# Performance work log

Hardware: AMD Instinct MI355X
Metric: run time of the kernel (lower is better)

The kernel has to match this reference:

```python
import jax, jax.numpy as jnp
import numpy as np

B, S, E, H = 2, 2048, 1024, 16
DH = E // H


def setup_inputs() -> dict:
    key = jax.random.key(0)
    ks = jax.random.split(key, 7)
    sc = 1.0 / np.sqrt(E)
    return {
        "x": jax.random.normal(ks[0], (B, S, E), dtype=jnp.float32),
        "Wq": jax.random.uniform(ks[1], (E, E), jnp.float32, -sc, sc),
        "bq": jax.random.uniform(ks[2], (E,), jnp.float32, -sc, sc),
        "Wk": jax.random.uniform(ks[3], (E, E), jnp.float32, -sc, sc),
        "bk": jax.random.uniform(ks[4], (E,), jnp.float32, -sc, sc),
        "Wv": jax.random.uniform(ks[5], (E, E), jnp.float32, -sc, sc),
        "bv": jax.random.uniform(ks[6], (E,), jnp.float32, -sc, sc),
    }


def reference(x, Wq, bq, Wk, bk, Wv, bv):
    b, s, _ = x.shape
    # torch Linear: y = x @ W.T + b
    q = (x @ Wq.T + bq).reshape(b, s, H, DH).transpose(0, 2, 1, 3)  # [B,H,S,Dh]
    k = (x @ Wk.T + bk).reshape(b, s, H, DH).transpose(0, 2, 1, 3)
    v = (x @ Wv.T + bv).reshape(b, s, H, DH).transpose(0, 2, 1, 3)
    # original einsum labels treat axis1 as 's' and axis2 as 'h'/'v':
    # scores: [B, S_q, H, S_k]  (softmax over keys, last axis)
    scores = jnp.einsum('bshd,bsvd->bhsv', q, k) / np.sqrt(DH)
    probs = jax.nn.softmax(scores, axis=-1)
    # out: [B, H, S, Dh] per original label permutation
    out = jnp.einsum('bhsv,bsvd->bshd', probs, v)
    # original reshapes WITHOUT transposing heads back (faithful quirk)
    return out.reshape(b, s, E)
```

## Files before the change

### kernel.cpp

```cpp
#include <hip/hip_runtime.h>
#include <hip/hip_bf16.h>

#define Bb 2
#define Ss 2048
#define Ee 1024
#define Hh 16
#define Dh 64
#define QSCALE 0.18033688011112042f

using u16 = unsigned short;
using u32 = unsigned int;
typedef __attribute__((ext_vector_type(8))) short short8;
typedef __attribute__((ext_vector_type(8))) u16 ushort8;
typedef __attribute__((ext_vector_type(4))) float f32x4;
typedef __attribute__((ext_vector_type(16))) float f32x16;
typedef __attribute__((ext_vector_type(4))) u32 uint4v;

#define GAS __attribute__((address_space(1)))
#define LAS __attribute__((address_space(3)))

__device__ __forceinline__ void gload16(const u16* g, u16* l) {
  __builtin_amdgcn_global_load_lds((const GAS unsigned int*)g,
                                   (LAS unsigned int*)l, 16, 0, 0);
}

__device__ __forceinline__ u16 f2bf(float f) {
  union { float f; unsigned u; } v;
  v.f = f;
  unsigned u = v.u;
  unsigned r = (u + 0x7FFFu + ((u >> 16) & 1u)) >> 16;
  return (u16)r;
}

__global__ __launch_bounds__(256) void cvt_all(
    const float* __restrict__ x, const float* __restrict__ wq,
    const float* __restrict__ wk, const float* __restrict__ wv,
    u16* __restrict__ xo, u16* __restrict__ wqo, u16* __restrict__ wko,
    u16* __restrict__ wvo) {
  const int b = blockIdx.x;
  const float* s;
  u16* d;
  int i;
  if (b < 2048) {
    s = x; d = xo; i = b * 256 + threadIdx.x;
  } else {
    const int wb = b - 2048;
    const int which = wb >> 9;
    s = which == 0 ? wq : (which == 1 ? wk : wv);
    d = which == 0 ? wqo : (which == 1 ? wko : wvo);
    i = (wb & 511) * 256 + threadIdx.x;
  }
  const float* p = s + (size_t)i * 8;
  ushort8 o;
#pragma unroll
  for (int j = 0; j < 8; ++j) o[j] = f2bf(p[j]);
  *(ushort8*)(d + (size_t)i * 8) = o;
}

__global__ __launch_bounds__(256) void qkv_gemm(
    const u16* __restrict__ Xb, const u16* __restrict__ Wcat,
    const float* __restrict__ bq, const float* __restrict__ bk,
    const float* __restrict__ bv,
    u16* __restrict__ Qo, u16* __restrict__ Ko, u16* __restrict__ Vo) {
  __shared__ u16 Ast[128][64];
  __shared__ u16 Bst[128][64];
  const int tid = threadIdx.x;
  const int lane = tid & 63;
  const int w = tid >> 6;
  const int wm = w >> 1, wn = w & 1;
  const int c = lane & 15, g = lane >> 4;
  const int m0 = blockIdx.y * 128;
  const int n0 = blockIdx.x * 128;
  const bool swapv = n0 >= 2048;

  f32x4 acc[4][4] = {};

  for (int kt = 0; kt < 16; ++kt) {
    const int k0 = kt * 64;
    __syncthreads();
#pragma unroll
    for (int i = 0; i < 4; ++i) {
      const int elem = i * 2048 + tid * 8;
      const int row = elem >> 6, col = elem & 63;
      const int lbase = i * 2048 + w * 512;
      gload16(Xb + (size_t)(m0 + row) * 1024 + k0 + col, &Ast[0][0] + lbase);
      gload16(Wcat + (size_t)(n0 + row) * 1024 + k0 + col, &Bst[0][0] + lbase);
    }
    __syncthreads();

#pragma unroll
    for (int ks = 0; ks < 2; ++ks) {
      short8 af[4], bf[4];
#pragma unroll
      for (int mf = 0; mf < 4; ++mf)
        af[mf] = *(const short8*)&Ast[wm * 64 + mf * 16 + c][ks * 32 + g * 8];
#pragma unroll
      for (int nf = 0; nf < 4; ++nf)
        bf[nf] = *(const short8*)&Bst[wn * 64 + nf * 16 + c][ks * 32 + g * 8];
      if (!swapv) {
#pragma unroll
        for (int mf = 0; mf < 4; ++mf)
#pragma unroll
          for (int nf = 0; nf < 4; ++nf)
            acc[mf][nf] = __builtin_amdgcn_mfma_f32_16x16x32_bf16(
                af[mf], bf[nf], acc[mf][nf], 0, 0, 0);
      } else {
#pragma unroll
        for (int mf = 0; mf < 4; ++mf)
#pragma unroll
          for (int nf = 0; nf < 4; ++nf)
            acc[mf][nf] = __builtin_amdgcn_mfma_f32_16x16x32_bf16(
                bf[nf], af[mf], acc[mf][nf], 0, 0, 0);
      }
    }
  }

  if (!swapv) {
    const int which = n0 >> 10;
    u16* Oo = which == 0 ? Qo : Ko;
    const float* bias = which == 0 ? bq : bk;
    const float scl = which == 0 ? QSCALE : 1.0f;
#pragma unroll
    for (int nf = 0; nf < 4; ++nf) {
      const int n = (n0 & 1023) + wn * 64 + nf * 16 + c;
      const float bval = bias[n];
      const int hh = n >> 6, dd = n & 63;
#pragma unroll
      for (int mf = 0; mf < 4; ++mf) {
#pragma unroll
        for (int r = 0; r < 4; ++r) {
          const int m = m0 + wm * 64 + mf * 16 + g * 4 + r;
          const int bb = m >> 11, ss = m & 2047;
          Oo[(((size_t)bb * Hh + hh) * Ss + ss) * Dh + dd] =
              f2bf((acc[mf][nf][r] + bval) * scl);
        }
      }
    }
  } else {
#pragma unroll
    for (int nf = 0; nf < 4; ++nf) {
#pragma unroll
      for (int r = 0; r < 4; ++r) {
        const int n = (n0 - 2048) + wn * 64 + nf * 16 + g * 4 + r;
        const float bval = bv[n];
        const int hh = n >> 6, dd = n & 63;
#pragma unroll
        for (int mf = 0; mf < 4; ++mf) {
          const int m = m0 + wm * 64 + mf * 16 + c;
          const int bb = m >> 11, ss = m & 2047;
          Vo[(((size_t)bb * Hh + hh) * Dh + dd) * Ss + ss] =
              f2bf(acc[mf][nf][r] + bval);
        }
      }
    }
  }
}

__global__ __launch_bounds__(256) void attn(
    const u16* __restrict__ Q, const u16* __restrict__ K,
    const u16* __restrict__ VT, float* __restrict__ out) {
  __shared__ u16 Kst[2][64][64];
  __shared__ u16 Vst[2][64][64];
  __shared__ float l_lds[4][32];
  const int tid = threadIdx.x;
  const int lane = tid & 63;
  const int w = tid >> 6;
  const int c5 = lane & 31, g2 = lane >> 5;
  const int bh = blockIdx.y;
  const int q0 = blockIdx.x * 128;
  const u16* Qb = Q + (size_t)bh * Ss * Dh;
  const u16* Kb = K + (size_t)bh * Ss * Dh;
  const u16* VTb = VT + (size_t)bh * Ss * Dh;

  const int srow = lane >> 3;
  const int scolx = ((lane & 7) * 8) ^ (srow * 8);

  const u16* Qrow = Qb + (size_t)(q0 + w * 32 + c5) * Dh + 8 * g2;
  short8 qf[4];
#pragma unroll
  for (int s = 0; s < 4; ++s) qf[s] = *(const short8*)(Qrow + 16 * s);

#pragma unroll
  for (int p = 0; p < 2; ++p) {
    const int row = w * 8 + srow + p * 32;
    gload16(Kb + (size_t)row * Dh + scolx, &Kst[0][0][0] + w * 512 + p * 2048);
    gload16(VTb + (size_t)row * Ss + scolx, &Vst[0][0][0] + w * 512 + p * 2048);
  }

  f32x16 oacc0 = {}, oacc1 = {};
  float lsum = 0.f;

  for (int kt = 0; kt < 32; ++kt) {
    __syncthreads();
    if (kt < 31) {
      const int k0n = (kt + 1) * 64;
      const int nb = (kt + 1) & 1;
#pragma unroll
      for (int p = 0; p < 2; ++p) {
        const int row = w * 8 + srow + p * 32;
        gload16(Kb + (size_t)(k0n + row) * Dh + scolx,
                &Kst[nb][0][0] + w * 512 + p * 2048);
        gload16(VTb + (size_t)row * Ss + k0n + scolx,
                &Vst[nb][0][0] + w * 512 + p * 2048);
      }
    }
    const char* kbuf = (const char*)&Kst[kt & 1][0][0];
    const char* vbuf = (const char*)&Vst[kt & 1][0][0];
    const int cxor = (c5 & 7) << 4;

    f32x16 sc0 = {}, sc1 = {};
    __builtin_amdgcn_s_setprio(1);
#pragma unroll
    for (int s = 0; s < 4; ++s) {
      const int cb = (32 * s + 16 * g2) ^ cxor;
      short8 kf0 = *(const short8*)(kbuf + c5 * 128 + cb);
      short8 kf1 = *(const short8*)(kbuf + (32 + c5) * 128 + cb);
      sc0 = __builtin_amdgcn_mfma_f32_32x32x16_bf16(kf0, qf[s], sc0, 0, 0, 0);
      sc1 = __builtin_amdgcn_mfma_f32_32x32x16_bf16(kf1, qf[s], sc1, 0, 0, 0);
    }
    __builtin_amdgcn_s_setprio(0);

    u32 pkv[2][8];
    float part = 0.f;
#pragma unroll
    for (int i = 0; i < 8; ++i) {
      const u32 e0 = __builtin_bit_cast(u32, __builtin_amdgcn_exp2f(sc0[2 * i]));
      const u32 e1 = __builtin_bit_cast(u32, __builtin_amdgcn_exp2f(sc0[2 * i + 1]));
      pkv[0][i] = (e0 >> 16) | (e1 & 0xFFFF0000u);
      part += __builtin_bit_cast(float, e0 & 0xFFFF0000u) +
              __builtin_bit_cast(float, e1 & 0xFFFF0000u);
    }
#pragma unroll
    for (int i = 0; i < 8; ++i) {
      const u32 e0 = __builtin_bit_cast(u32, __builtin_amdgcn_exp2f(sc1[2 * i]));
      const u32 e1 = __builtin_bit_cast(u32, __builtin_amdgcn_exp2f(sc1[2 * i + 1]));
      pkv[1][i] = (e0 >> 16) | (e1 & 0xFFFF0000u);
      part += __builtin_bit_cast(float, e0 & 0xFFFF0000u) +
              __builtin_bit_cast(float, e1 & 0xFFFF0000u);
    }
    lsum += part;

    __builtin_amdgcn_s_setprio(1);
#pragma unroll
    for (int sp = 0; sp < 4; ++sp) {
      const int kb = sp >> 1, sg = sp & 1;
      const u32 a0 = pkv[kb][4 * sg + 0], a1 = pkv[kb][4 * sg + 1];
      const u32 b0 = pkv[kb][4 * sg + 2], b1 = pkv[kb][4 * sg + 3];
      const u32 keep0 = g2 ? b0 : a0, keep1 = g2 ? b1 : a1;
      const u32 send0 = g2 ? a0 : b0, send1 = g2 ? a1 : b1;
      const u32 recv0 = (u32)__shfl_xor((int)send0, 32);
      const u32 recv1 = (u32)__shfl_xor((int)send1, 32);
      uint4v av;
      av[0] = g2 ? recv0 : keep0;
      av[1] = g2 ? recv1 : keep1;
      av[2] = g2 ? keep0 : recv0;
      av[3] = g2 ? keep1 : recv1;
      const short8 af = __builtin_bit_cast(short8, av);
      const int cb = (32 * sp + 16 * g2) ^ cxor;
      short8 vf0 = *(const short8*)(vbuf + c5 * 128 + cb);
      short8 vf1 = *(const short8*)(vbuf + (32 + c5) * 128 + cb);
      oacc0 = __builtin_amdgcn_mfma_f32_32x32x16_bf16(af, vf0, oacc0, 0, 0, 0);
      oacc1 = __builtin_amdgcn_mfma_f32_32x32x16_bf16(af, vf1, oacc1, 0, 0, 0);
    }
    __builtin_amdgcn_s_setprio(0);
  }

  float ltot = lsum + __shfl_xor(lsum, 32);
  if (g2 == 0) l_lds[w][c5] = ltot;
  asm volatile("s_waitcnt lgkmcnt(0)" ::: "memory");
  __builtin_amdgcn_sched_barrier(0);
  f32x4 lv[4];
#pragma unroll
  for (int t = 0; t < 4; ++t)
    lv[t] = *(const f32x4*)&l_lds[w][8 * t + 4 * g2];

  float* ob = out + (size_t)bh * Ss * Dh;
#pragma unroll
  for (int r = 0; r < 16; ++r) {
    const float inv = 1.0f / lv[r >> 2][r & 3];
    const int q = q0 + w * 32 + (r & 3) + 8 * (r >> 2) + 4 * g2;
    ob[(size_t)q * Dh + c5] = oacc0[r] * inv;
    ob[(size_t)q * Dh + 32 + c5] = oacc1[r] * inv;
  }
}

extern "C" void kernel_launch(void* const* d_in, const int* in_sizes, int n_in,
                              void* d_out, int out_size, void* d_ws, size_t ws_size,
                              hipStream_t stream) {
  const float* x = (const float*)d_in[0];
  const float* Wq = (const float*)d_in[1];
  const float* bq = (const float*)d_in[2];
  const float* Wk = (const float*)d_in[3];
  const float* bk = (const float*)d_in[4];
  const float* Wv = (const float*)d_in[5];
  const float* bv = (const float*)d_in[6];
  float* out = (float*)d_out;

  if (ws_size < (size_t)(38u << 20)) return;
  char* ws = (char*)d_ws;
  u16* Qb = (u16*)(ws + (size_t)(0u << 20));
  u16* Kb = (u16*)(ws + (size_t)(8u << 20));
  u16* Vb = (u16*)(ws + (size_t)(16u << 20));
  u16* Xb = (u16*)(ws + (size_t)(24u << 20));
  u16* Wqb = (u16*)(ws + (size_t)(32u << 20));
  u16* Wkb = (u16*)(ws + (size_t)(34u << 20));
  u16* Wvb = (u16*)(ws + (size_t)(36u << 20));

  cvt_all<<<3584, 256, 0, stream>>>(x, Wq, Wk, Wv, Xb, Wqb, Wkb, Wvb);
  qkv_gemm<<<dim3(24, 32), 256, 0, stream>>>(Xb, Wqb, bq, bk, bv, Qb, Kb, Vb);
  attn<<<dim3(16, 32), 256, 0, stream>>>(Qb, Kb, Vb, out);
}
```

Measured before the change: 113.0 us.

## Compute softmax row sums via MFMA with ones and use permlane32 swap

The softmax denominator is now accumulated by an extra MFMA that multiplies the probability fragment by a vector of bf16 ones. This replaces the per-element VALU adds and the final LDS reduction of row sums. The half-wave exchange uses v_permlane32_swap instead of shuffles and selects, and bf16 packing uses a byte permute. The grid is flattened and remapped so that consecutive blocks land on different (batch, head) pairs, likely for XCD/L2 locality. The trade is one extra MFMA per step, which adds matrix-core work.

```diff
diff --git a/kernel.cpp b/kernel.cpp
--- a/kernel.cpp
+++ b/kernel.cpp
@@ -161,13 +161,13 @@
     const u16* __restrict__ VT, float* __restrict__ out) {
   __shared__ u16 Kst[2][64][64];
   __shared__ u16 Vst[2][64][64];
-  __shared__ float l_lds[4][32];
   const int tid = threadIdx.x;
   const int lane = tid & 63;
   const int w = tid >> 6;
   const int c5 = lane & 31, g2 = lane >> 5;
-  const int bh = blockIdx.y;
-  const int q0 = blockIdx.x * 128;
+  const int flat = blockIdx.x;
+  const int bh = (flat & 7) * 4 + ((flat >> 3) >> 4);
+  const int q0 = ((flat >> 3) & 15) * 128;
   const u16* Qb = Q + (size_t)bh * Ss * Dh;
   const u16* Kb = K + (size_t)bh * Ss * Dh;
   const u16* VTb = VT + (size_t)bh * Ss * Dh;
@@ -179,6 +179,10 @@
   short8 qf[4];
 #pragma unroll
   for (int s = 0; s < 4; ++s) qf[s] = *(const short8*)(Qrow + 16 * s);
+
+  short8 ones;
+#pragma unroll
+  for (int j = 0; j < 8; ++j) ones[j] = (short)0x3F80;
 
 #pragma unroll
   for (int p = 0; p < 2; ++p) {
@@ -187,8 +191,7 @@
     gload16(VTb + (size_t)row * Ss + scolx, &Vst[0][0][0] + w * 512 + p * 2048);
   }
 
-  f32x16 oacc0 = {}, oacc1 = {};
-  float lsum = 0.f;
+  f32x16 oacc0 = {}, oacc1 = {}, lacc = {};
 
   for (int kt = 0; kt < 32; ++kt) {
     __syncthreads();
@@ -221,63 +224,44 @@
     __builtin_amdgcn_s_setprio(0);
 
     u32 pkv[2][8];
-    float part = 0.f;
 #pragma unroll
     for (int i = 0; i < 8; ++i) {
       const u32 e0 = __builtin_bit_cast(u32, __builtin_amdgcn_exp2f(sc0[2 * i]));
       const u32 e1 = __builtin_bit_cast(u32, __builtin_amdgcn_exp2f(sc0[2 * i + 1]));
-      pkv[0][i] = (e0 >> 16) | (e1 & 0xFFFF0000u);
-      part += __builtin_bit_cast(float, e0 & 0xFFFF0000u) +
-              __builtin_bit_cast(float, e1 & 0xFFFF0000u);
+      pkv[0][i] = __builtin_amdgcn_perm(e1, e0, 0x07060302u);
     }
 #pragma unroll
     for (int i = 0; i < 8; ++i) {
       const u32 e0 = __builtin_bit_cast(u32, __builtin_amdgcn_exp2f(sc1[2 * i]));
       const u32 e1 = __builtin_bit_cast(u32, __builtin_amdgcn_exp2f(sc1[2 * i + 1]));
-      pkv[1][i] = (e0 >> 16) | (e1 & 0xFFFF0000u);
-      part += __builtin_bit_cast(float, e0 & 0xFFFF0000u) +
-              __builtin_bit_cast(float, e1 & 0xFFFF0000u);
-    }
-    lsum += part;
+      pkv[1][i] = __builtin_amdgcn_perm(e1, e0, 0x07060302u);
+    }
 
     __builtin_amdgcn_s_setprio(1);
 #pragma unroll
     for (int sp = 0; sp < 4; ++sp) {
       const int kb = sp >> 1, sg = sp & 1;
-      const u32 a0 = pkv[kb][4 * sg + 0], a1 = pkv[kb][4 * sg + 1];
-      const u32 b0 = pkv[kb][4 * sg + 2], b1 = pkv[kb][4 * sg + 3];
-      const u32 keep0 = g2 ? b0 : a0, keep1 = g2 ? b1 : a1;
-      const u32 send0 = g2 ? a0 : b0, send1 = g2 ? a1 : b1;
-      const u32 recv0 = (u32)__shfl_xor((int)send0, 32);
-      const u32 recv1 = (u32)__shfl_xor((int)send1, 32);
+      u32 x0 = pkv[kb][4 * sg + 0], y0 = pkv[kb][4 * sg + 2];
+      u32 x1 = pkv[kb][4 * sg + 1], y1 = pkv[kb][4 * sg + 3];
+      asm("v_permlane32_swap_b32 %0, %1" : "+v"(x0), "+v"(y0));
+      asm("v_permlane32_swap_b32 %0, %1" : "+v"(x1), "+v"(y1));
       uint4v av;
-      av[0] = g2 ? recv0 : keep0;
-      av[1] = g2 ? recv1 : keep1;
-      av[2] = g2 ? keep0 : recv0;
-      av[3] = g2 ? keep1 : recv1;
+      av[0] = x0; av[1] = x1; av[2] = y0; av[3] = y1;
       const short8 af = __builtin_bit_cast(short8, av);
       const int cb = (32 * sp + 16 * g2) ^ cxor;
       short8 vf0 = *(const short8*)(vbuf + c5 * 128 + cb);
       short8 vf1 = *(const short8*)(vbuf + (32 + c5) * 128 + cb);
+      lacc = __builtin_amdgcn_mfma_f32_32x32x16_bf16(af, ones, lacc, 0, 0, 0);
       oacc0 = __builtin_amdgcn_mfma_f32_32x32x16_bf16(af, vf0, oacc0, 0, 0, 0);
       oacc1 = __builtin_amdgcn_mfma_f32_32x32x16_bf16(af, vf1, oacc1, 0, 0, 0);
     }
     __builtin_amdgcn_s_setprio(0);
   }
 
-  float ltot = lsum + __shfl_xor(lsum, 32);
-  if (g2 == 0) l_lds[w][c5] = ltot;
-  asm volatile("s_waitcnt lgkmcnt(0)" ::: "memory");
-  __builtin_amdgcn_sched_barrier(0);
-  f32x4 lv[4];
-#pragma unroll
-  for (int t = 0; t < 4; ++t)
-    lv[t] = *(const f32x4*)&l_lds[w][8 * t + 4 * g2];
-
   float* ob = out + (size_t)bh * Ss * Dh;
 #pragma unroll
   for (int r = 0; r < 16; ++r) {
-    const float inv = 1.0f / lv[r >> 2][r & 3];
+    const float inv = 1.0f / lacc[r];
     const int q = q0 + w * 32 + (r & 3) + 8 * (r >> 2) + 4 * g2;
     ob[(size_t)q * Dh + c5] = oacc0[r] * inv;
     ob[(size_t)q * Dh + 32 + c5] = oacc1[r] * inv;
@@ -308,5 +292,5 @@
 
   cvt_all<<<3584, 256, 0, stream>>>(x, Wq, Wk, Wv, Xb, Wqb, Wkb, Wvb);
   qkv_gemm<<<dim3(24, 32), 256, 0, stream>>>(Xb, Wqb, bq, bk, bv, Qb, Kb, Vb);
-  attn<<<dim3(16, 32), 256, 0, stream>>>(Qb, Kb, Vb, out);
-}
+  attn<<<512, 256, 0, stream>>>(Qb, Kb, Vb, out);
+}
```

Result: faster. 107.2 us (-5.2%).
